# Kernel optimization log

Measured on AMD Instinct MI355X. Metric: run time of the kernel, lower is better.

Reference implementation:

```python
import jax, jax.numpy as jnp
import numpy as np

T1, T2 = 10.0, 50.0          # Canny hysteresis thresholds from EdgeNorm
HYST_ITERS = 16              # fixed-iteration approximation of Canny hysteresis BFS
TEMPERATURE = 1.0
NUM_CLASSES_M1 = 13.0


def _shift(a, dy, dx):
    # zero-padded shift of [n,h,w]
    p = jnp.pad(a, ((0, 0), (1, 1), (1, 1)))
    return jax.lax.dynamic_slice(p, (0, 1 + dy, 1 + dx), a.shape)


def _sobel(img):
    # img: [n,h,w] float32; replicate border, aperture-3 Sobel (cv2.Canny default)
    p = jnp.pad(img, ((0, 0), (1, 1), (1, 1)), mode='edge')[:, None]  # [n,1,h+2,w+2]
    kx = jnp.array([[-1, 0, 1], [-2, 0, 2], [-1, 0, 1]], jnp.float32)
    ky = jnp.array([[-1, -2, -1], [0, 0, 0], [1, 2, 1]], jnp.float32)
    k = jnp.stack([kx, ky])[:, None]                                  # [2,1,3,3]
    g = jax.lax.conv_general_dilated(p, k, (1, 1), 'VALID')           # [n,2,h,w]
    return g[:, 0], g[:, 1]


def _canny(img_u8):
    # vectorized Canny over the batch (cv2 loops per sample on CPU)
    img = img_u8.astype(jnp.float32)
    gx, gy = _sobel(img)
    mag = jnp.abs(gx) + jnp.abs(gy)                 # L1 magnitude (cv2 L2gradient=False)
    ang = jnp.mod(jnp.degrees(jnp.arctan2(gy, gx)), 180.0)
    s0 = (ang < 22.5) | (ang >= 157.5)
    s45 = (ang >= 22.5) & (ang < 67.5)
    s90 = (ang >= 67.5) & (ang < 112.5)
    # non-max suppression: compare along quantized gradient direction
    n1 = jnp.where(s0, _shift(mag, 0, 1),
         jnp.where(s45, _shift(mag, -1, 1),
         jnp.where(s90, _shift(mag, -1, 0), _shift(mag, -1, -1))))
    n2 = jnp.where(s0, _shift(mag, 0, -1),
         jnp.where(s45, _shift(mag, 1, -1),
         jnp.where(s90, _shift(mag, 1, 0), _shift(mag, 1, 1))))
    nms = jnp.where((mag >= n1) & (mag >= n2), mag, 0.0)
    strong = nms > T2
    weak = nms > T1

    def body(_, s):
        grown = jax.lax.reduce_window(s.astype(jnp.float32), -jnp.inf, jax.lax.max,
                                      (1, 3, 3), (1, 1, 1),
                                      [(0, 0), (1, 1), (1, 1)]) > 0.0
        return grown & weak

    strong = jax.lax.fori_loop(0, HYST_ITERS, body, strong)
    return strong.astype(jnp.float32) * 255.0       # [n,h,w] in {0,255}


def _dilate_blur(edges):
    # cv2.dilate with 10x10 ones kernel, anchor=(5,5) -> asymmetric (5,4) window pad
    d = jax.lax.reduce_window(edges, -jnp.inf, jax.lax.max,
                              (1, 10, 10), (1, 1, 1),
                              [(0, 0), (5, 4), (5, 4)])
    # cv2.blur 10x10 box filter, reflect101 border, rounded back to uint8
    p = jnp.pad(d, ((0, 0), (5, 4), (5, 4)), mode='reflect')
    b = jax.lax.reduce_window(p, 0.0, jax.lax.add,
                              (1, 10, 10), (1, 1, 1), 'VALID') / 100.0
    return jnp.round(b) / 255.0                     # EdgeNorm: e / 255


def setup_inputs() -> dict:
    key = jax.random.key(0)
    k1, k2 = jax.random.split(key)
    n, c, h, w = 8, 14, 512, 512
    return {
        'preds_S': jax.random.normal(k1, (n, c, h, w), dtype=jnp.float32),
        'preds_T': jax.random.normal(k2, (n, c, h, w), dtype=jnp.float32),
    }


def reference(preds_S, preds_T):
    n, c, h, w = preds_S.shape
    # teacher argmax map -> uint8 grayscale (truncating cast, as torch .type(uint8))
    t_map = (jnp.argmax(preds_T, axis=1).astype(jnp.float32)
             / NUM_CLASSES_M1 * 255.0).astype(jnp.uint8)
    edges = jax.lax.stop_gradient(_dilate_blur(_canny(t_map)))  # [n,h,w], constant wrt grads
    pred_T = edges[:, None] * preds_T
    pred_S = edges[:, None] * preds_S
    # ChannelNorm: softmax over flattened h*w per (n,c); divergence='kl' -> norm_s.log()
    logsm_t = jax.nn.log_softmax(pred_T.reshape(n, c, h * w), axis=-1)
    logsm_s = jax.nn.log_softmax(pred_S.reshape(n, c, h * w), axis=-1)
    norm_t = jnp.exp(logsm_t)
    loss = jnp.sum(norm_t * (logsm_t - logsm_s))    # KLDivLoss(reduction='sum')
    loss = loss / (n * c)                           # channel norm divisor
    return loss * (TEMPERATURE ** 2)
```

## Files before the change

kernel.cpp:

```cpp
#include <hip/hip_runtime.h>
#include <math.h>

#define NB 8
#define CC 14
#define HH 512
#define WW 512
#define HW (HH*WW)
#define NHW (NB*HW)
#define WPR 8
#define WPI (HH*WPR)
#define KSPLIT 32
#define KCHUNK (HW/KSPLIT)

typedef unsigned long long u64;

__global__ __launch_bounds__(256) void k_argmax(const float* __restrict__ T,
                                                uchar4* __restrict__ tmap4) {
    int i4 = blockIdx.x * blockDim.x + threadIdx.x;
    if (i4 >= NHW / 4) return;
    int n  = i4 / (HW / 4);
    int p4 = i4 - n * (HW / 4);
    const float4* base = (const float4*)(T + (size_t)n * CC * HW) + p4;
    float4 best = base[0];
    int b0 = 0, b1 = 0, b2 = 0, b3 = 0;
#pragma unroll
    for (int c = 1; c < CC; ++c) {
        float4 v = base[(size_t)c * (HW / 4)];
        if (v.x > best.x) { best.x = v.x; b0 = c; }
        if (v.y > best.y) { best.y = v.y; b1 = c; }
        if (v.z > best.z) { best.z = v.z; b2 = c; }
        if (v.w > best.w) { best.w = v.w; b3 = c; }
    }
    uchar4 g;
    g.x = (unsigned char)(((float)b0 / 13.0f) * 255.0f);
    g.y = (unsigned char)(((float)b1 / 13.0f) * 255.0f);
    g.z = (unsigned char)(((float)b2 / 13.0f) * 255.0f);
    g.w = (unsigned char)(((float)b3 / 13.0f) * 255.0f);
    tmap4[i4] = g;
}

__global__ __launch_bounds__(256) void k_sobel_nms(const unsigned char* __restrict__ tmap,
                                                   u64* __restrict__ weakBits,
                                                   u64* __restrict__ strongBits) {
    int tx = blockIdx.x, ty = blockIdx.y, n = blockIdx.z;
    int x0 = tx * 64, y0 = ty * 64;
    __shared__ unsigned char tm[68 * 68];
    __shared__ unsigned short ms[66 * 66];
    int tid = threadIdx.x;
    const unsigned char* im = tmap + (size_t)n * HW;

    for (int idx = tid; idx < 68 * 68; idx += 256) {
        int r = idx / 68, c = idx - r * 68;
        int yy = y0 - 2 + r; yy = yy < 0 ? 0 : (yy > HH - 1 ? HH - 1 : yy);
        int xx = x0 - 2 + c; xx = xx < 0 ? 0 : (xx > WW - 1 ? WW - 1 : xx);
        tm[idx] = im[yy * WW + xx];
    }
    __syncthreads();

    for (int idx = tid; idx < 66 * 66; idx += 256) {
        int r = idx / 66, c = idx - r * 66;
        const unsigned char* t0 = tm + r * 68 + c;
        int a00 = t0[0],   a01 = t0[1],   a02 = t0[2];
        int a10 = t0[68],                 a12 = t0[70];
        int a20 = t0[136], a21 = t0[137], a22 = t0[138];
        int gx = (a02 - a00) + 2 * (a12 - a10) + (a22 - a20);
        int gy = (a20 - a00) + 2 * (a21 - a01) + (a22 - a02);
        int m = (gx < 0 ? -gx : gx) + (gy < 0 ? -gy : gy);
        float ang = atan2f((float)gy, (float)gx) * 57.29577951308232f;
        ang = fmodf(ang, 180.0f);
        if (ang < 0.0f) ang += 180.0f;
        int s;
        if (ang < 22.5f || ang >= 157.5f) s = 0;
        else if (ang < 67.5f)             s = 1;
        else if (ang < 112.5f)            s = 2;
        else                              s = 3;
        ms[idx] = (unsigned short)((m << 2) | s);
    }
    __syncthreads();

    int lane = tid & 63;
    int warp = tid >> 6;
#pragma unroll
    for (int it = 0; it < 16; ++it) {
        int row = it * 4 + warp;
        int gy_ = y0 + row, gx_ = x0 + lane;
        int v = ms[(row + 1) * 66 + (lane + 1)];
        int mc = v >> 2, s = v & 3;
        int dy1, dx1, dy2, dx2;
        if (s == 0)      { dy1 = 0;  dx1 = 1;  dy2 = 0; dx2 = -1; }
        else if (s == 1) { dy1 = -1; dx1 = 1;  dy2 = 1; dx2 = -1; }
        else if (s == 2) { dy1 = -1; dx1 = 0;  dy2 = 1; dx2 = 0;  }
        else             { dy1 = -1; dx1 = -1; dy2 = 1; dx2 = 1;  }
        int y1 = gy_ + dy1, x1 = gx_ + dx1, y2 = gy_ + dy2, x2 = gx_ + dx2;
        int n1 = (y1 < 0 || y1 >= HH || x1 < 0 || x1 >= WW)
                 ? 0 : (ms[(row + 1 + dy1) * 66 + (lane + 1 + dx1)] >> 2);
        int n2 = (y2 < 0 || y2 >= HH || x2 < 0 || x2 >= WW)
                 ? 0 : (ms[(row + 1 + dy2) * 66 + (lane + 1 + dx2)] >> 2);
        int nms = (mc >= n1 && mc >= n2) ? mc : 0;
        u64 wm = __ballot(nms > 10);
        u64 sm = __ballot(nms > 50);
        if (lane == 0) {
            size_t w = (size_t)n * WPI + gy_ * WPR + tx;
            weakBits[w]   = wm;
            strongBits[w] = sm;
        }
    }
}

#define HALO 21
#define TROWS (64 + 2*HALO)
#define TWORDS (TROWS * WPR)
__global__ __launch_bounds__(1024) void k_hyst_dil(const u64* __restrict__ strongBits,
                                                   const u64* __restrict__ weakBits,
                                                   u64* __restrict__ dilBits) {
    int tile = blockIdx.x & 7;
    int n    = blockIdx.x >> 3;
    int g0   = tile * 64 - HALO;
    __shared__ u64 A[TWORDS];
    __shared__ u64 B[TWORDS];
    __shared__ u64 Wl[TWORDS];
    int tid = threadIdx.x;

    if (tid < TWORDS) {
        int vr = g0 + (tid >> 3);
        int w  = tid & 7;
        u64 sv = 0, wv = 0;
        if (vr >= 0 && vr < HH) {
            sv = strongBits[(size_t)n * WPI + vr * WPR + w];
            wv = weakBits  [(size_t)n * WPI + vr * WPR + w];
        }
        A[tid] = sv;
        Wl[tid] = wv;
    }
    __syncthreads();

#pragma unroll 1
    for (int it = 0; it < 16; ++it) {
        const u64* src = (it & 1) ? B : A;
        u64*       dst = (it & 1) ? A : B;
        if (tid < TWORDS) {
            int r = tid >> 3;
            int w = tid & 7;
            u64 c  = src[tid];
            u64 up = (r > 0)         ? src[tid - 8] : 0;
            u64 dn = (r < TROWS - 1) ? src[tid + 8] : 0;
            u64 a = c | up | dn;
            u64 pL = 0, pR = 0;
            if (w > 0) {
                u64 cl = src[tid - 1];
                u64 ul = (r > 0)         ? src[tid - 9] : 0;
                u64 dl = (r < TROWS - 1) ? src[tid + 7] : 0;
                pL = cl | ul | dl;
            }
            if (w < 7) {
                u64 cr = src[tid + 1];
                u64 ur = (r > 0)         ? src[tid - 7] : 0;
                u64 dr = (r < TROWS - 1) ? src[tid + 9] : 0;
                pR = cr | ur | dr;
            }
            u64 g = a | (a << 1) | (pL >> 63) | (a >> 1) | (pR << 63);
            dst[tid] = g & Wl[tid];
        }
        __syncthreads();
    }

    if (tid < TWORDS) {
        int w = tid & 7;
        u64 v  = A[tid];
        u64 p  = (w > 0) ? A[tid - 1] : 0;
        u64 nx = (w < 7) ? A[tid + 1] : 0;
        u64 o = v;
#pragma unroll
        for (int d = 1; d <= 5; ++d) o |= (v << d) | (p >> (64 - d));
#pragma unroll
        for (int d = 1; d <= 4; ++d) o |= (v >> d) | (nx << (64 - d));
        B[tid] = o;
    }
    __syncthreads();

    if (tid < 64 * WPR) {
        int rr = tid >> 3;
        int w  = tid & 7;
        int r  = rr + HALO;
        u64 o = 0;
#pragma unroll
        for (int dy = -5; dy <= 4; ++dy) o |= B[(r + dy) * WPR + w];
        dilBits[(size_t)n * WPI + (tile * 64 + rr) * WPR + w] = o;
    }
}

__global__ __launch_bounds__(256) void k_blur(const u64* __restrict__ dilBits,
                                              float* __restrict__ E) {
    int n  = blockIdx.y;
    int y0 = blockIdx.x * 32;
    __shared__ u64 rows[42 * WPR];
    __shared__ unsigned char rc[42 * 512];
    int tid = threadIdx.x;

    for (int idx = tid; idx < 42 * WPR; idx += 256) {
        int vi = idx >> 3;
        int w  = idx & 7;
        int v  = y0 - 5 + vi;
        int r  = v < 0 ? -v : (v > HH - 1 ? 2 * (HH - 1) - v : v);
        rows[idx] = dilBits[(size_t)n * WPI + r * WPR + w];
    }
    __syncthreads();

    for (int idx = tid; idx < 42 * 512; idx += 256) {
        int r = idx >> 9;
        int x = idx & 511;
        int c;
        if (x >= 5 && x <= 507) {
            int b = x - 5, wd = b >> 6, off = b & 63;
            u64 v = rows[r * WPR + wd] >> off;
            if (off && wd < 7) v |= rows[r * WPR + wd + 1] << (64 - off);
            c = __popcll(v & 0x3FFull);
        } else {
            c = 0;
            for (int dx = -5; dx <= 4; ++dx) {
                int xx = x + dx;
                xx = xx < 0 ? -xx : (xx > WW - 1 ? 2 * (WW - 1) - xx : xx);
                c += (int)((rows[r * WPR + (xx >> 6)] >> (xx & 63)) & 1ull);
            }
        }
        rc[idx] = (unsigned char)c;
    }
    __syncthreads();

    for (int x = tid; x < 512; x += 256) {
        int sum = 0;
#pragma unroll
        for (int k = 0; k < 10; ++k) sum += rc[k * 512 + x];
        float* o = E + (size_t)n * HW + y0 * WW + x;
        o[0] = rintf((255.0f * (float)sum) / 100.0f) / 255.0f;
        for (int yy = 1; yy < 32; ++yy) {
            sum += (int)rc[(yy + 9) * 512 + x] - (int)rc[(yy - 1) * 512 + x];
            o[yy * WW] = rintf((255.0f * (float)sum) / 100.0f) / 255.0f;
        }
    }
}

__global__ __launch_bounds__(256) void k_kl_partial(const float* __restrict__ S,
                                                    const float* __restrict__ T,
                                                    const float* __restrict__ E,
                                                    double* __restrict__ partial) {
    int cidx  = blockIdx.x;
    int split = blockIdx.y;
    int n = cidx / CC;
    const float4* Tp = (const float4*)(T + (size_t)cidx * HW + (size_t)split * KCHUNK);
    const float4* Sp = (const float4*)(S + (size_t)cidx * HW + (size_t)split * KCHUNK);
    const float4* Ep = (const float4*)(E + (size_t)n    * HW + (size_t)split * KCHUNK);
    int tid = threadIdx.x;

    float Zt = 0.0f, Wt = 0.0f, Zs = 0.0f;
#pragma unroll
    for (int k = 0; k < KCHUNK / 4 / 256; ++k) {
        int j = k * 256 + tid;
        float4 t4 = Tp[j];
        float4 s4 = Sp[j];
        float4 e4 = Ep[j];
#pragma unroll
        for (int u = 0; u < 4; ++u) {
            float e = (&e4.x)[u];
            float t = e * (&t4.x)[u];
            float s = e * (&s4.x)[u];
            float et = __expf(t);
            Zt += et;
            Wt += et * (t - s);
            Zs += __expf(s);
        }
    }

    __shared__ double r1[256], r2[256], r3[256];
    r1[tid] = (double)Zt; r2[tid] = (double)Wt; r3[tid] = (double)Zs;
    __syncthreads();
    for (int off = 128; off > 0; off >>= 1) {
        if (tid < off) {
            r1[tid] += r1[tid + off];
            r2[tid] += r2[tid + off];
            r3[tid] += r3[tid + off];
        }
        __syncthreads();
    }
    if (tid == 0) {
        double* o = partial + ((size_t)cidx * KSPLIT + split) * 3;
        o[0] = r1[0]; o[1] = r2[0]; o[2] = r3[0];
    }
}

__global__ __launch_bounds__(128) void k_kl_final(const double* __restrict__ partial,
                                                  float* __restrict__ out) {
    int tid = threadIdx.x;
    double loss = 0.0;
    if (tid < NB * CC) {
        double Zt = 0.0, Wt = 0.0, Zs = 0.0;
        for (int sp = 0; sp < KSPLIT; ++sp) {
            const double* p = partial + ((size_t)tid * KSPLIT + sp) * 3;
            Zt += p[0]; Wt += p[1]; Zs += p[2];
        }
        loss = Wt / Zt - log(Zt) + log(Zs);
    }
    __shared__ double red[128];
    red[tid] = loss;
    __syncthreads();
    for (int off = 64; off > 0; off >>= 1) {
        if (tid < off) red[tid] += red[tid + off];
        __syncthreads();
    }
    if (tid == 0) out[0] = (float)(red[0] / (double)(NB * CC));
}

extern "C" void kernel_launch(void* const* d_in, const int* in_sizes, int n_in,
                              void* d_out, int out_size, void* d_ws, size_t ws_size,
                              hipStream_t stream) {
    const float* S = (const float*)d_in[0];
    const float* T = (const float*)d_in[1];
    float* out = (float*)d_out;

    char* ws = (char*)d_ws;
    float*         e_buf      = (float*)(ws);
    unsigned char* tmap       = (unsigned char*)(ws + (size_t)NHW * 4);
    u64*           weakBits   = (u64*)(ws + (size_t)NHW * 5);
    u64*           strongBits = (u64*)(ws + (size_t)NHW * 5 + (NHW/8));
    u64*           dilBits    = (u64*)(ws + (size_t)NHW * 5 + 2*(NHW/8));
    double*        partial    = (double*)(ws + (size_t)NHW * 5 + 3*(NHW/8));

    k_argmax<<<dim3(NHW / 4 / 256), dim3(256), 0, stream>>>(T, (uchar4*)tmap);
    k_sobel_nms<<<dim3(8, 8, NB), dim3(256), 0, stream>>>(tmap, weakBits, strongBits);
    k_hyst_dil<<<dim3(NB * 8), dim3(1024), 0, stream>>>(strongBits, weakBits, dilBits);
    k_blur<<<dim3(16, NB), dim3(256), 0, stream>>>(dilBits, e_buf);
    k_kl_partial<<<dim3(NB * CC, KSPLIT), dim3(256), 0, stream>>>(S, T, e_buf, partial);
    k_kl_final<<<1, 128, 0, stream>>>(partial, out);
    (void)in_sizes; (void)n_in; (void)out_size; (void)ws_size;
}
```

Baseline: 315.3 us.

## Fuse hysteresis/dilation with box blur kernel using wider halo

Merges the blur kernel into the hysteresis+dilation kernel. The halo grows from 21 to 26 rows so each tile can compute its dilated rows plus the 5/4-row blur neighbourhood locally. This removes the dilBits round trip through global memory and one kernel launch. In exchange it does more redundant halo work, uses more shared memory (an extra 37KB rc buffer), and replaces the per-column running sum with a direct 10-row sum per output.

```diff
diff --git a/kernel.cpp b/kernel.cpp
--- a/kernel.cpp
+++ b/kernel.cpp
@@ -107,18 +107,20 @@
     }
 }
 
-#define HALO 21
+#define HALO 26
 #define TROWS (64 + 2*HALO)
 #define TWORDS (TROWS * WPR)
-__global__ __launch_bounds__(1024) void k_hyst_dil(const u64* __restrict__ strongBits,
-                                                   const u64* __restrict__ weakBits,
-                                                   u64* __restrict__ dilBits) {
+__global__ __launch_bounds__(1024) void k_hyst_dil_blur(const u64* __restrict__ strongBits,
+                                                        const u64* __restrict__ weakBits,
+                                                        float* __restrict__ E) {
     int tile = blockIdx.x & 7;
     int n    = blockIdx.x >> 3;
-    int g0   = tile * 64 - HALO;
+    int t64  = tile * 64;
+    int g0   = t64 - HALO;
     __shared__ u64 A[TWORDS];
     __shared__ u64 B[TWORDS];
     __shared__ u64 Wl[TWORDS];
+    __shared__ unsigned char rc[74 * 512];
     int tid = threadIdx.x;
 
     if (tid < TWORDS) {
@@ -178,65 +180,57 @@
     }
     __syncthreads();
 
-    if (tid < 64 * WPR) {
-        int rr = tid >> 3;
-        int w  = tid & 7;
-        int r  = rr + HALO;
+    u64* D = Wl;
+    if (tid < 74 * WPR) {
+        int d = tid >> 3;
+        int w = tid & 7;
+        int r = d + 21;
         u64 o = 0;
 #pragma unroll
         for (int dy = -5; dy <= 4; ++dy) o |= B[(r + dy) * WPR + w];
-        dilBits[(size_t)n * WPI + (tile * 64 + rr) * WPR + w] = o;
-    }
-}
-
-__global__ __launch_bounds__(256) void k_blur(const u64* __restrict__ dilBits,
-                                              float* __restrict__ E) {
-    int n  = blockIdx.y;
-    int y0 = blockIdx.x * 32;
-    __shared__ u64 rows[42 * WPR];
-    __shared__ unsigned char rc[42 * 512];
-    int tid = threadIdx.x;
-
-    for (int idx = tid; idx < 42 * WPR; idx += 256) {
-        int vi = idx >> 3;
-        int w  = idx & 7;
-        int v  = y0 - 5 + vi;
-        int r  = v < 0 ? -v : (v > HH - 1 ? 2 * (HH - 1) - v : v);
-        rows[idx] = dilBits[(size_t)n * WPI + r * WPR + w];
-    }
-    __syncthreads();
-
-    for (int idx = tid; idx < 42 * 512; idx += 256) {
+        D[d * WPR + w] = o;
+    }
+    __syncthreads();
+
+    for (int idx = tid; idx < 74 * 512; idx += 1024) {
         int r = idx >> 9;
         int x = idx & 511;
         int c;
         if (x >= 5 && x <= 507) {
             int b = x - 5, wd = b >> 6, off = b & 63;
-            u64 v = rows[r * WPR + wd] >> off;
-            if (off && wd < 7) v |= rows[r * WPR + wd + 1] << (64 - off);
+            u64 v = D[r * WPR + wd] >> off;
+            if (off && wd < 7) v |= D[r * WPR + wd + 1] << (64 - off);
             c = __popcll(v & 0x3FFull);
         } else {
             c = 0;
             for (int dx = -5; dx <= 4; ++dx) {
                 int xx = x + dx;
                 xx = xx < 0 ? -xx : (xx > WW - 1 ? 2 * (WW - 1) - xx : xx);
-                c += (int)((rows[r * WPR + (xx >> 6)] >> (xx & 63)) & 1ull);
+                c += (int)((D[r * WPR + (xx >> 6)] >> (xx & 63)) & 1ull);
             }
         }
         rc[idx] = (unsigned char)c;
     }
     __syncthreads();
 
-    for (int x = tid; x < 512; x += 256) {
+    for (int idx = tid; idx < 64 * 512; idx += 1024) {
+        int yy = idx >> 9;
+        int x  = idx & 511;
+        int gy = t64 + yy;
         int sum = 0;
-#pragma unroll
-        for (int k = 0; k < 10; ++k) sum += rc[k * 512 + x];
-        float* o = E + (size_t)n * HW + y0 * WW + x;
-        o[0] = rintf((255.0f * (float)sum) / 100.0f) / 255.0f;
-        for (int yy = 1; yy < 32; ++yy) {
-            sum += (int)rc[(yy + 9) * 512 + x] - (int)rc[(yy - 1) * 512 + x];
-            o[yy * WW] = rintf((255.0f * (float)sum) / 100.0f) / 255.0f;
-        }
+        if (gy >= 5 && gy <= HH - 5) {
+#pragma unroll
+            for (int k = 0; k < 10; ++k) sum += rc[(yy + k) * 512 + x];
+        } else {
+#pragma unroll
+            for (int k = 0; k < 10; ++k) {
+                int v  = gy - 5 + k;
+                int rv = v < 0 ? -v : (v > HH - 1 ? 2 * (HH - 1) - v : v);
+                sum += rc[(rv - (t64 - 5)) * 512 + x];
+            }
+        }
+        float b = rintf((255.0f * (float)sum) / 100.0f);
+        E[(size_t)n * HW + gy * WW + x] = b / 255.0f;
     }
 }
 
@@ -322,13 +316,11 @@
     unsigned char* tmap       = (unsigned char*)(ws + (size_t)NHW * 4);
     u64*           weakBits   = (u64*)(ws + (size_t)NHW * 5);
     u64*           strongBits = (u64*)(ws + (size_t)NHW * 5 + (NHW/8));
-    u64*           dilBits    = (u64*)(ws + (size_t)NHW * 5 + 2*(NHW/8));
-    double*        partial    = (double*)(ws + (size_t)NHW * 5 + 3*(NHW/8));
+    double*        partial    = (double*)(ws + (size_t)NHW * 5 + 2*(NHW/8));
 
     k_argmax<<<dim3(NHW / 4 / 256), dim3(256), 0, stream>>>(T, (uchar4*)tmap);
     k_sobel_nms<<<dim3(8, 8, NB), dim3(256), 0, stream>>>(tmap, weakBits, strongBits);
-    k_hyst_dil<<<dim3(NB * 8), dim3(1024), 0, stream>>>(strongBits, weakBits, dilBits);
-    k_blur<<<dim3(16, NB), dim3(256), 0, stream>>>(dilBits, e_buf);
+    k_hyst_dil_blur<<<dim3(NB * 8), dim3(1024), 0, stream>>>(strongBits, weakBits, e_buf);
     k_kl_partial<<<dim3(NB * CC, KSPLIT), dim3(256), 0, stream>>>(S, T, e_buf, partial);
     k_kl_final<<<1, 128, 0, stream>>>(partial, out);
     (void)in_sizes; (void)n_in; (void)out_size; (void)ws_size;
```

New measurement: 301.4 us. 1.05x faster.
